# Kernel optimization log

Hardware: AMD Instinct MI355X
Metric: run time of the kernel (lower is better)

Reference implementation:

```python
import jax, jax.numpy as jnp
import numpy as np

N_NODES = 50000


def setup_inputs() -> dict:
    key = jax.random.key(0)
    k1, k2, k3, k4 = jax.random.split(key, 4)
    in_dim, out_dim, n_edges = 128, 64, 800000
    x = jax.random.normal(k1, (N_NODES, in_dim), dtype=jnp.float32)
    edge_index = jax.random.randint(k2, (2, n_edges), 0, N_NODES, dtype=jnp.int64)
    W = jax.random.normal(k3, (in_dim, out_dim), dtype=jnp.float32) * (1.0 / np.sqrt(in_dim))
    att = jax.random.normal(k4, (2 * out_dim,), dtype=jnp.float32) * (1.0 / np.sqrt(2 * out_dim))
    return {"x": x, "edge_index": edge_index, "W": W, "att": att}


def reference(x, edge_index, W, att):
    N = x.shape[0]
    F_out = W.shape[1]
    h = x @ W                                   # [N, F]
    src, dst = edge_index[0], edge_index[1]
    hs = h[src]                                 # [E, F] gather
    hd = h[dst]                                 # [E, F] gather
    # att(cat([h_src, h_dst])) == h_src @ a1 + h_dst @ a2
    a1, a2 = att[:F_out], att[F_out:]
    logit = jax.nn.leaky_relu(hs @ a1 + hd @ a2, 0.2)   # [E]
    E = logit.shape[0]
    # The original builds a dense [N, E] matrix (row d holds logit_e at col e
    # for dst[e]==d, zeros elsewhere) and softmaxes over the E axis. The
    # equivalent sparse form: denom_d = sum_{e:dst=d} exp(logit_e) + (E - deg_d)*exp(0),
    # stabilized with m_d = max(max logit over segment, 0).
    seg_max = jax.ops.segment_max(logit, dst, num_segments=N)      # -inf on empty
    m = jnp.maximum(seg_max, 0.0)                                  # include the zero cells
    exp_l = jnp.exp(logit - m[dst])                                # [E]
    seg_sum = jax.ops.segment_sum(exp_l, dst, num_segments=N)      # [N]
    deg = jax.ops.segment_sum(jnp.ones_like(logit), dst, num_segments=N)
    denom = seg_sum + (jnp.float32(E) - deg) * jnp.exp(-m)         # zeros' contribution
    w = exp_l / denom[dst]                                          # [E]
    agg = jax.ops.segment_sum(w[:, None] * hs, dst, num_segments=N)  # [N, F]
    return jax.nn.elu(agg)
```

## Files before the change

kernel.cpp:

```cpp
#include <hip/hip_runtime.h>
#include <hip/hip_bf16.h>

#define FIN 128
#define FOUT 64
#define BINW 128
#define NBINPAD 512
#define QS 2560
#define TILE 4096
#define DPQ 32
#define RCAP 768

typedef __attribute__((ext_vector_type(8))) short short8;
typedef __attribute__((ext_vector_type(4))) float f32x4;

__device__ __forceinline__ unsigned short f2bf(float f) {
    unsigned u = __float_as_uint(f);
    unsigned r = u + 0x7FFFu + ((u >> 16) & 1u);
    return (unsigned short)(r >> 16);
}

__global__ __launch_bounds__(256) void k_prep(
    const float* __restrict__ W, const float* __restrict__ att,
    unsigned short* __restrict__ Whig, unsigned short* __restrict__ Wlog,
    float* __restrict__ wag, int* __restrict__ qcur, int nzero)
{
    const int t = threadIdx.x;
    if (blockIdx.x >= 65) {
        const int i = (blockIdx.x - 65) * 256 + t;
        if (i < nzero) qcur[i] = 0;
        return;
    }
    if (blockIdx.x == 64) {
        const int k = t & 127, which = t >> 7;
        const float* av = att + which * 64;
        const float* wr = W + k * 64;
        float acc = 0.f;
        #pragma unroll 16
        for (int n = 0; n < 64; ++n) acc += wr[n] * av[n];
        wag[which * 128 + k] = acc;
        return;
    }
    const int f = blockIdx.x * 256 + t;
    const int combo = f >> 9;
    const int s = combo >> 2, c = combo & 3;
    const int r = f & 511;
    const int l = r >> 3, j = r & 7;
    const int k = s * 32 + (l >> 4) * 8 + j;
    const int n = c * 16 + (l & 15);
    const float w = W[k * 64 + n];
    const unsigned short hi = f2bf(w);
    const float hif = __uint_as_float((unsigned)hi << 16);
    Whig[f] = hi;
    Wlog[f] = f2bf(w - hif);
}

__global__ __launch_bounds__(256) void k_fused(
    const float* __restrict__ x, const unsigned short* __restrict__ Whig,
    const unsigned short* __restrict__ Wlog, const float* __restrict__ wag,
    unsigned* __restrict__ h2, float* __restrict__ as_, float* __restrict__ ad_,
    const int* __restrict__ src, const int* __restrict__ dst,
    unsigned* __restrict__ queue, int* __restrict__ qcur,
    int N, int E, int nbins, int paBlocks)
{
    union SMem {
        struct { unsigned rec[TILE]; int hist[NBINPAD]; int scanb[NBINPAD];
                 int comb[NBINPAD]; } pa;
    };
    __shared__ SMem sm;
    const int t = threadIdx.x;

    if ((int)blockIdx.x < paBlocks) {
        const int e0 = blockIdx.x * TILE;
        const int tot = (E - e0 < TILE) ? (E - e0) : TILE;
        sm.pa.hist[t] = 0; sm.pa.hist[t + 256] = 0;
        __syncthreads();
        #pragma unroll
        for (int i = 0; i < TILE / 256; ++i) {
            const int e = e0 + i * 256 + t;
            if (e < E) atomicAdd(&sm.pa.hist[__builtin_nontemporal_load(dst + e) >> 7], 1);
        }
        __syncthreads();
        const int v0 = sm.pa.hist[t], v1 = sm.pa.hist[t + 256];
        sm.pa.scanb[t] = v0; sm.pa.scanb[t + 256] = v1;
        __syncthreads();
        #pragma unroll
        for (int off = 1; off < NBINPAD; off <<= 1) {
            const int a0 = (t >= off) ? sm.pa.scanb[t - off] : 0;
            const int a1 = (t + 256 >= off) ? sm.pa.scanb[t + 256 - off] : 0;
            __syncthreads();
            sm.pa.scanb[t] += a0; sm.pa.scanb[t + 256] += a1;
            __syncthreads();
        }
        const int ex0 = sm.pa.scanb[t] - v0;
        const int ex1 = sm.pa.scanb[t + 256] - v1;
        int c0 = 0, c1 = 0;
        if (t < nbins && v0 > 0)
            c0 = t * QS + atomicAdd(qcur + t, v0) - ex0;
        if (t + 256 < nbins && v1 > 0)
            c1 = (t + 256) * QS + atomicAdd(qcur + t + 256, v1) - ex1;
        sm.pa.hist[t] = ex0; sm.pa.hist[t + 256] = ex1;
        sm.pa.comb[t] = c0;  sm.pa.comb[t + 256] = c1;
        __syncthreads();
        #pragma unroll
        for (int i = 0; i < TILE / 256; ++i) {
            const int e = e0 + i * 256 + t;
            if (e < E) {
                const int d = __builtin_nontemporal_load(dst + e);
                const int s = __builtin_nontemporal_load(src + e);
                const int pos = atomicAdd(&sm.pa.hist[d >> 7], 1);
                sm.pa.rec[pos] = (unsigned)s | ((unsigned)d << 16);
            }
        }
        __syncthreads();
        for (int i = t; i < tot; i += 256) {
            const unsigned r = sm.pa.rec[i];
            const int b = (int)(r >> 23);
            const int gpos = sm.pa.comb[b] + i;
            if (gpos < (b + 1) * QS)
                __builtin_nontemporal_store(r, queue + gpos);
        }
        return;
    }

    const int bb = blockIdx.x - paBlocks;
    const int wv = t >> 6, lane = t & 63;
    const int quad = lane >> 4, mrow = lane & 15;
    const int r0 = (bb * 4 + wv) * 16;
    const int arow = r0 + mrow;
    const bool rok = arow < N;

    f32x4 acc[4] = {};
    float s1 = 0.f, s2 = 0.f;

    #pragma unroll
    for (int s = 0; s < 4; ++s) {
        float xv[8];
        if (rok) {
            const float4* p = (const float4*)(x + (size_t)arow * FIN + s * 32 + quad * 8);
            const float4 u0 = p[0], u1 = p[1];
            xv[0] = u0.x; xv[1] = u0.y; xv[2] = u0.z; xv[3] = u0.w;
            xv[4] = u1.x; xv[5] = u1.y; xv[6] = u1.z; xv[7] = u1.w;
        } else {
            #pragma unroll
            for (int j = 0; j < 8; ++j) xv[j] = 0.f;
        }
        const float4 wa0 = *(const float4*)&wag[s * 32 + quad * 8];
        const float4 wa1 = *(const float4*)&wag[s * 32 + quad * 8 + 4];
        const float4 wb0 = *(const float4*)&wag[128 + s * 32 + quad * 8];
        const float4 wb1 = *(const float4*)&wag[128 + s * 32 + quad * 8 + 4];
        const float wva[8] = {wa0.x, wa0.y, wa0.z, wa0.w, wa1.x, wa1.y, wa1.z, wa1.w};
        const float wvb[8] = {wb0.x, wb0.y, wb0.z, wb0.w, wb1.x, wb1.y, wb1.z, wb1.w};

        short8 ah, al;
        #pragma unroll
        for (int j = 0; j < 8; ++j) {
            s1 += xv[j] * wva[j];
            s2 += xv[j] * wvb[j];
            const unsigned short hi = f2bf(xv[j]);
            const float hif = __uint_as_float((unsigned)hi << 16);
            ah[j] = (short)hi;
            al[j] = (short)f2bf(xv[j] - hif);
        }
        #pragma unroll
        for (int c = 0; c < 4; ++c) {
            const short8 bh = *(const short8*)&Whig[((s * 4 + c) * 64 + lane) * 8];
            const short8 bl = *(const short8*)&Wlog[((s * 4 + c) * 64 + lane) * 8];
            acc[c] = __builtin_amdgcn_mfma_f32_16x16x32_bf16(ah, bh, acc[c], 0, 0, 0);
            acc[c] = __builtin_amdgcn_mfma_f32_16x16x32_bf16(al, bh, acc[c], 0, 0, 0);
            acc[c] = __builtin_amdgcn_mfma_f32_16x16x32_bf16(ah, bl, acc[c], 0, 0, 0);
        }
    }

    s1 += __shfl_xor(s1, 16); s1 += __shfl_xor(s1, 32);
    s2 += __shfl_xor(s2, 16); s2 += __shfl_xor(s2, 32);
    if (lane < 16 && r0 + lane < N) {
        as_[r0 + lane] = s1;
        ad_[r0 + lane] = s2;
    }

    #pragma unroll
    for (int reg = 0; reg < 4; ++reg) {
        const int orow = r0 + quad * 4 + reg;
        if (orow < N) {
            #pragma unroll
            for (int c = 0; c < 2; ++c) {
                const unsigned lo = (unsigned)__builtin_bit_cast(unsigned short,
                                        (_Float16)acc[c][reg]);
                const unsigned hi = (unsigned)__builtin_bit_cast(unsigned short,
                                        (_Float16)acc[c + 2][reg]);
                h2[(size_t)orow * 32 + c * 16 + mrow] = lo | (hi << 16);
            }
        }
    }
}

__global__ __launch_bounds__(256) void k_aggq(
    const int* __restrict__ qcur, const unsigned* __restrict__ queue,
    const float* __restrict__ as_, const float* __restrict__ ad_,
    const unsigned* __restrict__ h2, float* __restrict__ out,
    int N, float Ef)
{
    __shared__ unsigned rec[RCAP];
    __shared__ unsigned pay[RCAP];
    __shared__ float wexp[RCAP];
    __shared__ int hist[DPQ], base[DPQ], cur[DPQ];
    __shared__ float adl[DPQ];
    __shared__ int nloc;

    const int bin = blockIdx.x >> 2, q = blockIdx.x & 3;
    const int d0 = bin * BINW + q * DPQ;
    const int t = threadIdx.x;
    const int wv = t >> 6, lane = t & 63;

    if (t < DPQ) {
        hist[t] = 0;
        const int d = d0 + t;
        adl[t] = (d < N) ? ad_[d] : 0.f;
    }
    if (t == 0) nloc = 0;
    __syncthreads();

    int cnt = qcur[bin];
    if (cnt > QS) cnt = QS;

    for (int i = t; i < cnt; i += 256) {
        const unsigned r = __builtin_nontemporal_load(queue + (size_t)bin * QS + i);
        const bool m = ((int)((r >> 21) & 3) == q);
        const unsigned long long mk = __ballot(m);
        int b0 = 0;
        if (lane == 0 && mk) b0 = atomicAdd(&nloc, __popcll(mk));
        b0 = __shfl(b0, 0);
        if (m) {
            const int p = b0 + __popcll(mk & ((1ull << lane) - 1ull));
            if (p < RCAP) {
                rec[p] = r;
                atomicAdd(&hist[(r >> 16) & (DPQ - 1)], 1);
            }
        }
    }
    __syncthreads();
    int n = nloc; if (n > RCAP) n = RCAP;

    if (t < DPQ) base[t] = hist[t];
    __syncthreads();
    #pragma unroll
    for (int off = 1; off < DPQ; off <<= 1) {
        const int a = (t < DPQ && t >= off) ? base[t - off] : 0;
        __syncthreads();
        if (t < DPQ) base[t] += a;
        __syncthreads();
    }
    if (t < DPQ) { base[t] -= hist[t]; cur[t] = base[t]; }
    __syncthreads();

    for (int i = t; i < n; i += 256) {
        const unsigned r = rec[i];
        const int s  = (int)(r & 0xFFFFu);
        const int dl = (int)(r >> 16) & (DPQ - 1);
        const float z = as_[s] + adl[dl];
        const float lg = (z >= 0.f) ? z : 0.2f * z;
        const int pos = atomicAdd(&cur[dl], 1);
        pay[pos] = (unsigned)s |
            ((unsigned)__builtin_bit_cast(unsigned short, (_Float16)lg) << 16);
    }
    __syncthreads();

    const int e2 = lane >> 5, pl = lane & 31;
    for (int dl = wv; dl < DPQ; dl += 4) {
        const int d = d0 + dl;
        if (d >= N) continue;
        const int dg = hist[dl];
        const int bs = base[dl];

        float mx = -INFINITY;
        for (int j = lane; j < dg; j += 64)
            mx = fmaxf(mx, (float)__builtin_bit_cast(_Float16,
                          (unsigned short)(pay[bs + j] >> 16)));
        #pragma unroll
        for (int off = 32; off > 0; off >>= 1) mx = fmaxf(mx, __shfl_xor(mx, off));
        const float m = fmaxf(mx, 0.f);

        float ss = 0.f;
        for (int j = lane; j < dg; j += 64) {
            const float e = expf((float)__builtin_bit_cast(_Float16,
                       (unsigned short)(pay[bs + j] >> 16)) - m);
            wexp[bs + j] = e;
            ss += e;
        }
        #pragma unroll
        for (int off = 32; off > 0; off >>= 1) ss += __shfl_xor(ss, off);
        const float inv = 1.f / (ss + (Ef - (float)dg) * expf(-m));

        float a0 = 0.f, a1 = 0.f;
        for (int jb = 0; jb < dg; jb += 16) {
            float w[8]; int s[8];
            #pragma unroll
            for (int u = 0; u < 8; ++u) {
                const int j = jb + u * 2 + e2;
                if (j < dg) {
                    s[u] = (int)(pay[bs + j] & 0xFFFFu);
                    w[u] = wexp[bs + j] * inv;
                } else { s[u] = 0; w[u] = 0.f; }
            }
            #pragma unroll
            for (int u = 0; u < 8; ++u) {
                const unsigned hp = h2[(size_t)s[u] * 32 + pl];
                const float h0 = (float)__builtin_bit_cast(_Float16,
                                     (unsigned short)(hp & 0xFFFFu));
                const float h1 = (float)__builtin_bit_cast(_Float16,
                                     (unsigned short)(hp >> 16));
                a0 += w[u] * h0;
                a1 += w[u] * h1;
            }
        }
        a0 += __shfl_xor(a0, 32);
        a1 += __shfl_xor(a1, 32);

        if (lane < 32) {
            const float r0v = (a0 > 0.f) ? a0 : expm1f(a0);
            const float r1v = (a1 > 0.f) ? a1 : expm1f(a1);
            out[(size_t)d * FOUT + pl] = r0v;
            out[(size_t)d * FOUT + 32 + pl] = r1v;
        }
    }
}

extern "C" void kernel_launch(void* const* d_in, const int* in_sizes, int n_in,
                              void* d_out, int out_size, void* d_ws, size_t ws_size,
                              hipStream_t stream) {
    const float* x   = (const float*)d_in[0];
    const int*   ei  = (const int*)d_in[1];
    const float* W   = (const float*)d_in[2];
    const float* att = (const float*)d_in[3];

    const int N = in_sizes[0] / FIN;
    const int E = in_sizes[1] / 2;
    const int* src = ei;
    const int* dst = ei + E;

    const int NBINS = (N + BINW - 1) / BINW;

    char* ws = (char*)d_ws;
    size_t o = 0;
    auto carve = [&](size_t bytes) {
        void* p = ws + o; o += (bytes + 1023) & ~(size_t)1023; return p;
    };
    unsigned short* Whig = (unsigned short*)carve(16384 * 2);
    unsigned short* Wlog = (unsigned short*)carve(16384 * 2);
    float*          wag  = (float*)carve(256 * 4);
    float*          as_  = (float*)carve((size_t)N * 4);
    float*          ad_  = (float*)carve((size_t)N * 4);
    int*            qcur = (int*)carve((size_t)NBINS * 4);
    unsigned*       h2   = (unsigned*)carve((size_t)N * 32 * 4);
    unsigned*       queue = (unsigned*)carve((size_t)NBINS * QS * 4);

    float* out = (float*)d_out;

    const int paBlocks = (E + TILE - 1) / TILE;
    const int mmBlocks = (N + 63) / 64;
    const int zBlks    = (NBINS + 255) / 256;

    k_prep<<<65 + zBlks, 256, 0, stream>>>(W, att, Whig, Wlog, wag, qcur, NBINS);
    k_fused<<<paBlocks + mmBlocks, 256, 0, stream>>>(
        x, Whig, Wlog, wag, h2, as_, ad_, src, dst, queue, qcur, N, E, NBINS, paBlocks);
    k_aggq<<<NBINS * 4, 256, 0, stream>>>(qcur, queue, as_, ad_, h2, out, N, (float)E);
}
```

Measured before the change: 142.8 us.

## Assign each destination to a 16-lane group instead of a full wave

```diff
diff --git a/kernel.cpp b/kernel.cpp
--- a/kernel.cpp
+++ b/kernel.cpp
@@ -17,6 +17,13 @@
     unsigned u = __float_as_uint(f);
     unsigned r = u + 0x7FFFu + ((u >> 16) & 1u);
     return (unsigned short)(r >> 16);
+}
+
+__device__ __forceinline__ float f16lo(unsigned u) {
+    return (float)__builtin_bit_cast(_Float16, (unsigned short)(u & 0xFFFFu));
+}
+__device__ __forceinline__ float f16hi(unsigned u) {
+    return (float)__builtin_bit_cast(_Float16, (unsigned short)(u >> 16));
 }
 
 __global__ __launch_bounds__(256) void k_prep(
@@ -265,38 +272,43 @@
     }
     __syncthreads();
 
-    const int e2 = lane >> 5, pl = lane & 31;
-    for (int dl = wv; dl < DPQ; dl += 4) {
+    const int grp = lane >> 4, ln = lane & 15;
+    const int g16 = wv * 4 + grp;
+    #pragma unroll
+    for (int k = 0; k < 2; ++k) {
+        const int dl = g16 + k * 16;
         const int d = d0 + dl;
-        if (d >= N) continue;
-        const int dg = hist[dl];
-        const int bs = base[dl];
+        const bool ok = (d < N);
+        const int dg = ok ? hist[dl] : 0;
+        const int bs = ok ? base[dl] : 0;
 
         float mx = -INFINITY;
-        for (int j = lane; j < dg; j += 64)
-            mx = fmaxf(mx, (float)__builtin_bit_cast(_Float16,
-                          (unsigned short)(pay[bs + j] >> 16)));
-        #pragma unroll
-        for (int off = 32; off > 0; off >>= 1) mx = fmaxf(mx, __shfl_xor(mx, off));
+        for (int j = ln; j < dg; j += 16)
+            mx = fmaxf(mx, f16hi(pay[bs + j]));
+        mx = fmaxf(mx, __shfl_xor(mx, 8, 16));
+        mx = fmaxf(mx, __shfl_xor(mx, 4, 16));
+        mx = fmaxf(mx, __shfl_xor(mx, 2, 16));
+        mx = fmaxf(mx, __shfl_xor(mx, 1, 16));
         const float m = fmaxf(mx, 0.f);
 
         float ss = 0.f;
-        for (int j = lane; j < dg; j += 64) {
-            const float e = expf((float)__builtin_bit_cast(_Float16,
-                       (unsigned short)(pay[bs + j] >> 16)) - m);
+        for (int j = ln; j < dg; j += 16) {
+            const float e = expf(f16hi(pay[bs + j]) - m);
             wexp[bs + j] = e;
             ss += e;
         }
-        #pragma unroll
-        for (int off = 32; off > 0; off >>= 1) ss += __shfl_xor(ss, off);
+        ss += __shfl_xor(ss, 8, 16);
+        ss += __shfl_xor(ss, 4, 16);
+        ss += __shfl_xor(ss, 2, 16);
+        ss += __shfl_xor(ss, 1, 16);
         const float inv = 1.f / (ss + (Ef - (float)dg) * expf(-m));
 
-        float a0 = 0.f, a1 = 0.f;
-        for (int jb = 0; jb < dg; jb += 16) {
+        float a00 = 0.f, a01 = 0.f, a10 = 0.f, a11 = 0.f;
+        for (int jb = 0; jb < dg; jb += 8) {
             float w[8]; int s[8];
             #pragma unroll
             for (int u = 0; u < 8; ++u) {
-                const int j = jb + u * 2 + e2;
+                const int j = jb + u;
                 if (j < dg) {
                     s[u] = (int)(pay[bs + j] & 0xFFFFu);
                     w[u] = wexp[bs + j] * inv;
@@ -304,23 +316,23 @@
             }
             #pragma unroll
             for (int u = 0; u < 8; ++u) {
-                const unsigned hp = h2[(size_t)s[u] * 32 + pl];
-                const float h0 = (float)__builtin_bit_cast(_Float16,
-                                     (unsigned short)(hp & 0xFFFFu));
-                const float h1 = (float)__builtin_bit_cast(_Float16,
-                                     (unsigned short)(hp >> 16));
-                a0 += w[u] * h0;
-                a1 += w[u] * h1;
-            }
-        }
-        a0 += __shfl_xor(a0, 32);
-        a1 += __shfl_xor(a1, 32);
-
-        if (lane < 32) {
-            const float r0v = (a0 > 0.f) ? a0 : expm1f(a0);
-            const float r1v = (a1 > 0.f) ? a1 : expm1f(a1);
-            out[(size_t)d * FOUT + pl] = r0v;
-            out[(size_t)d * FOUT + 32 + pl] = r1v;
+                const uint2 hp = *(const uint2*)&h2[(size_t)s[u] * 32 + 2 * ln];
+                a00 += w[u] * f16lo(hp.x);
+                a01 += w[u] * f16hi(hp.x);
+                a10 += w[u] * f16lo(hp.y);
+                a11 += w[u] * f16hi(hp.y);
+            }
+        }
+
+        if (ok) {
+            const float r00 = (a00 > 0.f) ? a00 : expm1f(a00);
+            const float r10 = (a10 > 0.f) ? a10 : expm1f(a10);
+            const float r01 = (a01 > 0.f) ? a01 : expm1f(a01);
+            const float r11 = (a11 > 0.f) ? a11 : expm1f(a11);
+            float2* op0 = (float2*)(out + (size_t)d * FOUT + 2 * ln);
+            float2* op1 = (float2*)(out + (size_t)d * FOUT + 32 + 2 * ln);
+            *op0 = make_float2(r00, r10);
+            *op1 = make_float2(r01, r11);
         }
     }
 }
```

After: 129.1 us. 9.6% less time.
